# Kernel optimization log

Hardware: AMD Instinct MI355X
Metric: run time of the kernel (lower is better)

The kernel has to match this reference:

```python
import jax, jax.numpy as jnp
import numpy as np
import math

NUM_BITS = 8
EPS = 1e-5


def fake_quant(x, num_bits=NUM_BITS):
    """Uniform fake quantization over the tensor's full range (min/max), STE-friendly."""
    qmax = 2.0 ** num_bits - 1.0
    mn = jnp.min(x)
    mx = jnp.max(x)
    scale = jnp.maximum((mx - mn) / qmax, 1e-8)
    q = jnp.round(jnp.clip((x - mn) / scale, 0.0, qmax)) * scale + mn
    # straight-through estimator: forward = q, backward = identity
    return x + jax.lax.stop_gradient(q - x)


def qconv(x, w, stride, pad):
    """QConv2d: fake-quantize input (8b) and weight (8b), then fp conv (no bias)."""
    return jax.lax.conv_general_dilated(
        fake_quant(x), fake_quant(w),
        window_strides=(stride, stride),
        padding=[(pad, pad), (pad, pad)],
        dimension_numbers=("NCHW", "OIHW", "NCHW"))


def range_norm(x, gamma, beta):
    """RangeN / RangeBN (Banner et al.): per-channel mean subtraction and
    range-based scale (max-min over N,H,W) with the Gaussian range correction
    factor; affine params with 8-bit fake-quantized gamma."""
    B, C, H, W = x.shape
    n = B * H * W  # elements per channel
    scale_fix = (0.5 * 0.35) * (1.0 + (math.pi * math.log(4.0)) ** 0.5) / ((2.0 * math.log(n)) ** 0.5)
    mean = jnp.mean(x, axis=(0, 2, 3), keepdims=True)          # [1,C,1,1]
    xc = x - mean
    rng = jnp.max(xc, axis=(0, 2, 3), keepdims=True) - jnp.min(xc, axis=(0, 2, 3), keepdims=True)
    out = xc / (rng * scale_fix + EPS)
    qg = fake_quant(gamma)
    return out * qg[None, :, None, None] + beta[None, :, None, None]


def qsum(a, b):
    """Qsum: fake-quantize both addends to 8 bits, then add."""
    return fake_quant(a) + fake_quant(b)


def setup_inputs() -> dict:
    key = jax.random.key(0)
    ks = jax.random.split(key, 4)
    B, Cin, H, W = 64, 1024, 14, 14
    P = 256  # planes; expansion 4 -> Cout = 1024 == Cin (identity residual)
    x = jax.random.normal(ks[0], (B, Cin, H, W), jnp.float32)
    w1 = jax.random.normal(ks[1], (P, Cin, 1, 1), jnp.float32) * (1.0 / math.sqrt(Cin))
    w2 = jax.random.normal(ks[2], (P, P, 3, 3), jnp.float32) * (1.0 / math.sqrt(P * 9))
    w3 = jax.random.normal(ks[3], (4 * P, P, 1, 1), jnp.float32) * (1.0 / math.sqrt(P))
    g1 = jnp.ones((P,), jnp.float32); b1 = jnp.zeros((P,), jnp.float32)
    g2 = jnp.ones((P,), jnp.float32); b2 = jnp.zeros((P,), jnp.float32)
    g3 = jnp.ones((4 * P,), jnp.float32); b3 = jnp.zeros((4 * P,), jnp.float32)
    return {"x": x, "w1": w1, "g1": g1, "b1": b1, "w2": w2, "g2": g2, "b2": b2,
            "w3": w3, "g3": g3, "b3": b3}


def reference(x, w1, g1, b1, w2, g2, b2, w3, g3, b3):
    out = qconv(x, w1, stride=1, pad=0)
    out = range_norm(out, g1, b1)
    out = qconv(out, w2, stride=1, pad=1)
    out = range_norm(out, g2, b2)
    out = qconv(out, w3, stride=1, pad=0)
    out = range_norm(out, g3, b3)
    return qsum(x, out)  # downsample is None -> identity residual
```

## Files before the change

kernel.cpp:

```cpp
#include <hip/hip_runtime.h>
#include <math.h>

#ifndef M_PI
#define M_PI 3.14159265358979323846
#endif

#define NB   64
#define NCOL 12544

typedef __attribute__((ext_vector_type(4))) int int4v;

static const size_t OF_OUT = 0;
static const size_t OF_XC  = 3211264;
static const size_t OF_Z1P = 6422528;
static const size_t OF_Z2C = 7471104;
static const size_t OF_WQ1 = 8273920;
static const size_t OF_WQ2 = 8339456;
static const size_t OF_WQ3 = 8486912;
static const size_t OF_R1  = 8552448;
static const size_t OF_R2  = 8552704;
static const size_t OF_R3  = 8552960;
static const size_t OF_T2  = 8553984;
static const size_t OF_CX  = 8556032;
static const size_t OF_U2  = 8568576;
static const size_t OF_V2  = 8584960;
static const size_t OF_CZ  = 8597504;
static const size_t OF_P1  = 8610048;
static const size_t OF_P2  = 8685312;
static const size_t OF_P3  = 8760576;
static const size_t OF_PMM = 9061632;
static const size_t OF_RS  = 9064192;
static const size_t OF_ST  = 9068800;
static const size_t OF_MS  = 9068864;

__device__ __forceinline__ float fqv(float v, float mn, float sc) {
    float t = (v - mn) / sc;
    t = fminf(fmaxf(t, 0.0f), 255.0f);
    return rintf(t) * sc + mn;
}
__device__ __forceinline__ float codef(float v, float mn, float sc) {
    float t = (v - mn) / sc;
    t = fminf(fmaxf(t, 0.0f), 255.0f);
    return rintf(t) - 128.0f;
}
__device__ __forceinline__ unsigned short f2bf(float f) { return (unsigned short)(__float_as_uint(f) >> 16); }
__device__ __forceinline__ float bf2f(unsigned short u) { return __uint_as_float(((unsigned)u) << 16); }
__device__ __forceinline__ int pack4(float a, float b, float c, float d) {
    return (int)(unsigned char)(signed char)(int)a | ((int)(unsigned char)(signed char)(int)b << 8) |
           ((int)(unsigned char)(signed char)(int)c << 16) | ((int)(unsigned char)(signed char)(int)d << 24);
}
__device__ __forceinline__ void glds16(const void* g, void* l) {
    __builtin_amdgcn_global_load_lds((const __attribute__((address_space(1))) unsigned int*)g,
                                     (__attribute__((address_space(3))) unsigned int*)l, 16, 0, 0);
}

__global__ __launch_bounds__(256) void k_minmax_all(const float4* __restrict__ x, const float4* __restrict__ w1,
                                                    const float4* __restrict__ w2, const float4* __restrict__ w3,
                                                    float* __restrict__ Pmm) {
    int b = blockIdx.x;
    const float4* p; int lb, nb, n4, base;
    if (b < 1024)      { p = x;  lb = b;        nb = 1024; n4 = 3211264; base = 0; }
    else if (b < 1088) { p = w1; lb = b - 1024; nb = 64;   n4 = 65536;   base = 2048; }
    else if (b < 1216) { p = w2; lb = b - 1088; nb = 128;  n4 = 147456;  base = 2176; }
    else               { p = w3; lb = b - 1216; nb = 64;   n4 = 65536;   base = 2432; }
    float mn = INFINITY, mx = -INFINITY;
    for (int i = lb * 256 + threadIdx.x; i < n4; i += nb * 256) {
        float4 v = p[i];
        mn = fminf(mn, fminf(fminf(v.x, v.y), fminf(v.z, v.w)));
        mx = fmaxf(mx, fmaxf(fmaxf(v.x, v.y), fmaxf(v.z, v.w)));
    }
    for (int o = 32; o; o >>= 1) {
        mn = fminf(mn, __shfl_down(mn, o, 64));
        mx = fmaxf(mx, __shfl_down(mx, o, 64));
    }
    __shared__ float smn[4], smx[4];
    int lane = threadIdx.x & 63, w = threadIdx.x >> 6;
    if (lane == 0) { smn[w] = mn; smx[w] = mx; }
    __syncthreads();
    if (threadIdx.x == 0) {
        for (int i = 1; i < 4; i++) { mn = fminf(mn, smn[i]); mx = fmaxf(mx, smx[i]); }
        Pmm[base + lb * 2]     = mn;
        Pmm[base + lb * 2 + 1] = mx;
    }
}

__global__ __launch_bounds__(256) void k_fqparams2(const float* __restrict__ Pmm, float* __restrict__ sf) {
    __shared__ float sa[4], sb[4];
    int t = threadIdx.x, lane = t & 63, w = t >> 6;
    const int nbs[4]   = {1024, 64, 128, 64};
    const int bases[4] = {0, 2048, 2176, 2432};
    for (int ten = 0; ten < 4; ten++) {
        float mn = INFINITY, mx = -INFINITY;
        for (int i = t; i < nbs[ten]; i += 256) {
            mn = fminf(mn, Pmm[bases[ten] + 2 * i]);
            mx = fmaxf(mx, Pmm[bases[ten] + 2 * i + 1]);
        }
        for (int o = 32; o; o >>= 1) {
            mn = fminf(mn, __shfl_down(mn, o, 64));
            mx = fmaxf(mx, __shfl_down(mx, o, 64));
        }
        if (lane == 0) { sa[w] = mn; sb[w] = mx; }
        __syncthreads();
        if (t == 0) {
            mn = fminf(fminf(sa[0], sa[1]), fminf(sa[2], sa[3]));
            mx = fmaxf(fmaxf(sb[0], sb[1]), fmaxf(sb[2], sb[3]));
            sf[8 + 3 * ten] = mn;
            sf[9 + 3 * ten] = fmaxf((mx - mn) / 255.0f, 1e-8f);
        }
        __syncthreads();
    }
}

__global__ __launch_bounds__(256) void k_wcode_all(const float* __restrict__ w1, const float* __restrict__ w2,
                                                   const float* __restrict__ w3, const float* __restrict__ sf,
                                                   signed char* __restrict__ wq1, signed char* __restrict__ wq2,
                                                   signed char* __restrict__ wq3,
                                                   float* __restrict__ R1, float* __restrict__ R2,
                                                   float* __restrict__ R3, float* __restrict__ T8) {
    __shared__ float sh[64];
    int b = blockIdx.x, t = threadIdx.x;
    int lane = t & 63, wv = t >> 6;
    if (b < 1280) {
        const float* w; signed char* wc; float* R; int K, co; const float* pw;
        if (b < 256) { w = w1; wc = wq1; R = R1; K = 1024; co = b; pw = sf + 11; }
        else         { w = w3; wc = wq3; R = R3; K = 256;  co = b - 256; pw = sf + 17; }
        float mn = pw[0], s = pw[1];
        float sum = 0.f;
        for (int k0 = t * 4; k0 < K; k0 += 1024) {
            float4 v = *(const float4*)&w[(size_t)co * K + k0];
            float c0 = codef(v.x, mn, s), c1 = codef(v.y, mn, s), c2 = codef(v.z, mn, s), c3 = codef(v.w, mn, s);
            *(int*)&wc[(size_t)co * K + k0] = pack4(c0, c1, c2, c3);
            sum += c0 + c1 + c2 + c3;
        }
        for (int o = 32; o; o >>= 1) sum += __shfl_down(sum, o, 64);
        if (lane == 0) sh[wv] = sum;
        __syncthreads();
        if (t == 0) R[co] = sh[0] + sh[1] + sh[2] + sh[3];
    } else {
        int co = b - 1280, ci = t;
        float mn = sf[14], s = sf[15];
        float tp[9];
#pragma unroll
        for (int p = 0; p < 9; p++) {
            float c = codef(w2[((size_t)co * 256 + ci) * 9 + p], mn, s);
            wq2[(size_t)co * 2304 + p * 256 + ci] = (signed char)(int)c;
            tp[p] = c;
        }
        float* red = sh;
        float* sT = sh + 40;
#pragma unroll
        for (int p = 0; p < 9; p++) {
            float v = tp[p];
            for (int o = 32; o; o >>= 1) v += __shfl_down(v, o, 64);
            if (lane == 0) red[wv * 9 + p] = v;
        }
        __syncthreads();
        if (ci < 9) sT[ci] = red[ci] + red[9 + ci] + red[18 + ci] + red[27 + ci];
        __syncthreads();
        if (ci == 0) {
            float T0 = sT[0], T1 = sT[1], T2 = sT[2], T3 = sT[3],
                  T5 = sT[5], T6 = sT[6], T7 = sT[7], T8v = sT[8];
            R2[co] = T0 + T1 + T2 + T3 + sT[4] + T5 + T6 + T7 + T8v;
            float* o = &T8[co * 8];
            o[0] = T0 + T1 + T2;
            o[1] = T6 + T7 + T8v;
            o[2] = T0 + T3 + T6;
            o[3] = T2 + T5 + T8v;
            o[4] = T0; o[5] = T2; o[6] = T6; o[7] = T8v;
        }
    }
}

__global__ __launch_bounds__(256) void k_code0(const float* __restrict__ x, signed char* __restrict__ dst,
                                               const float* __restrict__ qp, float* __restrict__ CX) {
    __shared__ unsigned short lt[28][264];
    int n = blockIdx.z, hw0 = blockIdx.x * 28, cq = blockIdx.y * 256;
    int t = threadIdx.x;
    float qmn = qp[0], qsc = qp[1];
    const float* sp = x + ((size_t)n * 1024 + cq) * 196 + hw0;
    for (int i = t; i < 7168; i += 256) {
        int c = i / 28, hw = i - c * 28;
        lt[hw][c] = f2bf(codef(sp[(size_t)c * 196 + hw], qmn, qsc));
    }
    __syncthreads();
    int lane = t & 63, wv = t >> 6;
    int c0 = lane * 4;
#pragma unroll
    for (int s = 0; s < 7; s++) {
        int i = s * 4 + wv;
        int pk = pack4(bf2f(lt[i][c0]), bf2f(lt[i][c0 + 1]), bf2f(lt[i][c0 + 2]), bf2f(lt[i][c0 + 3]));
        *(int*)&dst[((size_t)n * 196 + hw0 + i) * 1024 + cq + c0] = pk;
    }
    for (int i = wv; i < 28; i += 4) {
        float s = bf2f(lt[i][lane]) + bf2f(lt[i][lane + 64]) +
                  bf2f(lt[i][lane + 128]) + bf2f(lt[i][lane + 192]);
        for (int o = 32; o; o >>= 1) s += __shfl_down(s, o, 64);
        if (lane == 0) atomicAdd(&CX[n * 196 + hw0 + i], s);
    }
}

template <int PAD>
__global__ __launch_bounds__(256) void k_codeE(const float* __restrict__ src, signed char* __restrict__ dst,
                                               const float* __restrict__ mean, const float* __restrict__ sg,
                                               const float* __restrict__ beta, const float* __restrict__ qp,
                                               float* __restrict__ rowsum) {
    int t = threadIdx.x, lane = t & 63, wv = t >> 6;
    int c4 = lane * 4;
    float4 m4 = *(const float4*)&mean[c4];
    float4 s4 = *(const float4*)&sg[c4];
    float4 b4 = *(const float4*)&beta[c4];
    float qmn = qp[0], qsc = qp[1];
#pragma unroll
    for (int r = 0; r < 4; r++) {
        int j = blockIdx.x * 16 + wv * 4 + r;
        float4 v = *(const float4*)&src[(size_t)j * 256 + c4];
        float c0 = codef((v.x - m4.x) * s4.x + b4.x, qmn, qsc);
        float c1 = codef((v.y - m4.y) * s4.y + b4.y, qmn, qsc);
        float c2 = codef((v.z - m4.z) * s4.z + b4.z, qmn, qsc);
        float c3 = codef((v.w - m4.w) * s4.w + b4.w, qmn, qsc);
        int n = j / 196, hw = j - n * 196, h = hw / 14, w = hw - (hw / 14) * 14;
        size_t di;
        if (PAD) di = (((size_t)n * 16 + h + 1) * 16 + (w + 1)) * 256 + c4;
        else     di = (size_t)j * 256 + c4;
        *(int*)&dst[di] = pack4(c0, c1, c2, c3);
        float s = c0 + c1 + c2 + c3;
        for (int o = 32; o; o >>= 1) s += __shfl_down(s, o, 64);
        if (lane == 0) {
            if (PAD) rowsum[((size_t)n * 16 + h + 1) * 16 + (w + 1)] = s;
            else     rowsum[j] = s;
        }
    }
}

__global__ __launch_bounds__(256) void k_v2(const float* __restrict__ U, float* __restrict__ V) {
    int j = blockIdx.x * 256 + threadIdx.x;
    if (j >= NCOL) return;
    int n = j / 196, hw = j - n * 196, h = hw / 14, w = hw - (hw / 14) * 14;
    const float* u = U + (size_t)n * 256;
    float s = 0.f;
#pragma unroll
    for (int r = 0; r < 3; r++)
#pragma unroll
        for (int c = 0; c < 3; c++) s += u[(h + r) * 16 + (w + c)];
    V[j] = s;
}

template <int MODE>
__global__ __launch_bounds__(256, 2) void k_conv12(const signed char* __restrict__ Acts,
                                                   const signed char* __restrict__ Wts,
                                                   const float* __restrict__ R, const float* __restrict__ T8,
                                                   const float* __restrict__ Cj,
                                                   const float* __restrict__ pw, const float* __restrict__ pz,
                                                   float* __restrict__ outNHWC, int K,
                                                   float* __restrict__ Ps, float* __restrict__ Pn,
                                                   float* __restrict__ Px) {
    __shared__ __align__(16) signed char As[2 * 16384];
    __shared__ __align__(16) signed char Bs[2 * 8192];
    __shared__ float Lst[2][64][3];
    int tid = threadIdx.x, lane = tid & 63, wave = tid >> 6;
    int wm = wave >> 1, wn = wave & 1;
    int jb = blockIdx.x * 128, cob = blockIdx.y * 64;
    int sr = tid >> 3, spos = tid & 7, sc = spos ^ (sr & 7);

    const signed char* aq[4];
#pragma unroll
    for (int q = 0; q < 4; q++) {
        int j = jb + q * 32 + sr;
        if (MODE == 0) aq[q] = Acts + (size_t)j * K + sc * 16;
        else {
            int n = j / 196, hw = j - n * 196, h = hw / 14, w = hw - (hw / 14) * 14;
            aq[q] = Acts + (((size_t)n * 16 + h) * 16 + w) * 256 + sc * 16;
        }
    }
    const signed char* bq[2];
#pragma unroll
    for (int q = 0; q < 2; q++) bq[q] = Wts + (size_t)(cob + q * 32 + sr) * K + sc * 16;

    int4v acc[4][2];
#pragma unroll
    for (int mi = 0; mi < 4; mi++)
#pragma unroll
        for (int ni = 0; ni < 2; ni++) acc[mi][ni] = (int4v)0;

    int nk = K >> 7;
    auto stage = [&](int b, int ks) {
        size_t koA;
        if (MODE == 0) koA = (size_t)ks << 7;
        else {
            int k = ks << 7;
            int p = k >> 8, kin = k & 255;
            int rr = p / 3, ss = p - 3 * rr;
            koA = (size_t)(rr * 16 + ss) * 256 + kin;
        }
#pragma unroll
        for (int q = 0; q < 4; q++)
            glds16(aq[q] + koA, &As[b * 16384 + (q * 32 + sr) * 128 + spos * 16]);
#pragma unroll
        for (int q = 0; q < 2; q++)
            glds16(bq[q] + ((size_t)ks << 7), &Bs[b * 8192 + (q * 32 + sr) * 128 + spos * 16]);
    };

    int l15 = lane & 15, kq = lane >> 4, sw = l15 & 7;
    stage(0, 0);
    for (int ks = 0; ks < nk; ks++) {
        __syncthreads();
        if (ks + 1 < nk) stage((ks + 1) & 1, ks + 1);
        int b = ks & 1;
#pragma unroll
        for (int kc = 0; kc < 2; kc++) {
            int col = ((kc * 4 + kq) ^ sw) << 4;
            int4v a[4], bb[2];
#pragma unroll
            for (int mi = 0; mi < 4; mi++)
                a[mi] = *(const int4v*)&As[b * 16384 + (wm * 64 + mi * 16 + l15) * 128 + col];
#pragma unroll
            for (int ni = 0; ni < 2; ni++)
                bb[ni] = *(const int4v*)&Bs[b * 8192 + (wn * 32 + ni * 16 + l15) * 128 + col];
#pragma unroll
            for (int mi = 0; mi < 4; mi++)
#pragma unroll
                for (int ni = 0; ni < 2; ni++)
                    acc[mi][ni] = __builtin_amdgcn_mfma_i32_16x16x64_i8(a[mi], bb[ni], acc[mi][ni], 0, 0, 0);
        }
    }

    float aw = pw[1], bw = pw[0] + 128.f * pw[1];
    float az = pz[1], bz = pz[0] + 128.f * pz[1];
    float caa = aw * az, cR = aw * bz, cC = bw * az, cK = bw * bz;
    int cco[2]; float rr0[2]; float t8v[2][8];
#pragma unroll
    for (int ni = 0; ni < 2; ni++) {
        cco[ni] = cob + wn * 32 + ni * 16 + l15;
        rr0[ni] = R[cco[ni]];
        if (MODE == 1) {
#pragma unroll
            for (int p = 0; p < 8; p++) t8v[ni][p] = T8[cco[ni] * 8 + p];
        }
    }
    float ssm[2] = {0.f, 0.f}, smnv[2] = {INFINITY, INFINITY}, smxv[2] = {-INFINITY, -INFINITY};
#pragma unroll
    for (int mi = 0; mi < 4; mi++)
#pragma unroll
        for (int reg = 0; reg < 4; reg++) {
            int j = jb + wm * 64 + mi * 16 + kq * 4 + reg;
            int n = j / 196, hw = j - n * 196;
            float cj = Cj[j];
            float constterm;
            float pt = 0.f, pb = 0.f, pl = 0.f, pr = 0.f, ctl = 0.f, ctr = 0.f, cbl = 0.f, cbr = 0.f;
            if (MODE == 1) {
                int h = hw / 14, w = hw - (hw / 14) * 14;
                pt = (h == 0) ? 1.f : 0.f;  pb = (h == 13) ? 1.f : 0.f;
                pl = (w == 0) ? 1.f : 0.f;  pr = (w == 13) ? 1.f : 0.f;
                ctl = pt * pl; ctr = pt * pr; cbl = pb * pl; cbr = pb * pr;
                float miss = 3.f * (pt + pb + pl + pr) - (ctl + ctr + cbl + cbr);
                constterm = cK * (256.f * (9.f - miss));
            } else {
                constterm = cK * (float)K;
            }
#pragma unroll
            for (int ni = 0; ni < 2; ni++) {
                float rsum = rr0[ni];
                if (MODE == 1)
                    rsum -= pt * t8v[ni][0] + pb * t8v[ni][1] + pl * t8v[ni][2] + pr * t8v[ni][3]
                          - ctl * t8v[ni][4] - ctr * t8v[ni][5] - cbl * t8v[ni][6] - cbr * t8v[ni][7];
                float v = caa * (float)acc[mi][ni][reg] + cR * rsum + cC * cj + constterm;
                outNHWC[(size_t)j * 256 + cco[ni]] = v;
                ssm[ni] += v;
                smnv[ni] = fminf(smnv[ni], v);
                smxv[ni] = fmaxf(smxv[ni], v);
            }
        }
#pragma unroll
    for (int ni = 0; ni < 2; ni++) {
        float s = ssm[ni], mn = smnv[ni], mx = smxv[ni];
        s += __shfl_xor(s, 16, 64); s += __shfl_xor(s, 32, 64);
        mn = fminf(mn, __shfl_xor(mn, 16, 64)); mn = fminf(mn, __shfl_xor(mn, 32, 64));
        mx = fmaxf(mx, __shfl_xor(mx, 16, 64)); mx = fmaxf(mx, __shfl_xor(mx, 32, 64));
        if (kq == 0) {
            int cl = wn * 32 + ni * 16 + l15;
            Lst[wm][cl][0] = s; Lst[wm][cl][1] = mn; Lst[wm][cl][2] = mx;
        }
    }
    __syncthreads();
    if (tid < 64) {
        float s  = Lst[0][tid][0] + Lst[1][tid][0];
        float mn = fminf(Lst[0][tid][1], Lst[1][tid][1]);
        float mx = fmaxf(Lst[0][tid][2], Lst[1][tid][2]);
        int idx = blockIdx.x * 256 + cob + tid;
        Ps[idx] = s; Pn[idx] = mn; Px[idx] = mx;
    }
}

__global__ __launch_bounds__(256, 2) void k_conv3(const signed char* __restrict__ Wts,
                                                  const signed char* __restrict__ Zc,
                                                  const float* __restrict__ R, const float* __restrict__ Cj,
                                                  const float* __restrict__ pw, const float* __restrict__ pz,
                                                  float* __restrict__ out,
                                                  float* __restrict__ Ps, float* __restrict__ Pn,
                                                  float* __restrict__ Px) {
    __shared__ __align__(16) signed char As[32768];
    __shared__ __align__(16) signed char Bs[32768];
    __shared__ float Lst[2][128][3];
    int tid = threadIdx.x, lane = tid & 63, wave = tid >> 6;
    int wm = wave >> 1, wn = wave & 1;
    int jb = blockIdx.x * 128, cob = blockIdx.y * 128;
    int sr = tid >> 4, spos = tid & 15;
#pragma unroll
    for (int p = 0; p < 8; p++) {
        int row = p * 16 + sr;
        int cg = spos ^ (row & 7);
        glds16(Zc + (size_t)(jb + row) * 256 + cg * 16, &As[p * 4096 + tid * 16]);
    }
#pragma unroll
    for (int p = 0; p < 8; p++) {
        int row = p * 16 + sr;
        int cg = spos ^ (row & 7);
        glds16(Wts + (size_t)(cob + row) * 256 + cg * 16, &Bs[p * 4096 + tid * 16]);
    }
    __syncthreads();

    int4v acc[4][4];
#pragma unroll
    for (int mi = 0; mi < 4; mi++)
#pragma unroll
        for (int ni = 0; ni < 4; ni++) acc[mi][ni] = (int4v)0;

    int l15 = lane & 15, kq = lane >> 4, sw = l15 & 7;
#pragma unroll
    for (int kc = 0; kc < 4; kc++) {
        int col = ((kc * 4 + kq) ^ sw) << 4;
        int4v a[4], bb[4];
#pragma unroll
        for (int mi = 0; mi < 4; mi++)
            a[mi] = *(const int4v*)&As[(wm * 64 + mi * 16 + l15) * 256 + col];
#pragma unroll
        for (int ni = 0; ni < 4; ni++)
            bb[ni] = *(const int4v*)&Bs[(wn * 64 + ni * 16 + l15) * 256 + col];
#pragma unroll
        for (int mi = 0; mi < 4; mi++)
#pragma unroll
            for (int ni = 0; ni < 4; ni++)
                acc[mi][ni] = __builtin_amdgcn_mfma_i32_16x16x64_i8(a[mi], bb[ni], acc[mi][ni], 0, 0, 0);
    }

    float aw = pw[1], bw = pw[0] + 128.f * pw[1];
    float az = pz[1], bz = pz[0] + 128.f * pz[1];
    float caa = aw * az, cR = aw * bz, cC = bw * az, cK = bw * bz;
    int coA[4]; float rA[4];
#pragma unroll
    for (int ni = 0; ni < 4; ni++) {
        coA[ni] = cob + wn * 64 + ni * 16 + l15;
        rA[ni] = R[coA[ni]];
    }
    float ps[4], pmn[4], pmx[4];
#pragma unroll
    for (int ni = 0; ni < 4; ni++) { ps[ni] = 0.f; pmn[ni] = INFINITY; pmx[ni] = -INFINITY; }
#pragma unroll
    for (int mi = 0; mi < 4; mi++) {
        int j0 = jb + wm * 64 + mi * 16 + kq * 4;
        int n = j0 / 196, hh = j0 - n * 196;
        float4 cj = *(const float4*)&Cj[j0];
#pragma unroll
        for (int ni = 0; ni < 4; ni++) {
            float base = cR * rA[ni] + cK * 256.f;
            float4 v;
            v.x = caa * (float)acc[mi][ni][0] + base + cC * cj.x;
            v.y = caa * (float)acc[mi][ni][1] + base + cC * cj.y;
            v.z = caa * (float)acc[mi][ni][2] + base + cC * cj.z;
            v.w = caa * (float)acc[mi][ni][3] + base + cC * cj.w;
            *(float4*)&out[((size_t)n * 1024 + coA[ni]) * 196 + hh] = v;
            ps[ni] += v.x + v.y + v.z + v.w;
            pmn[ni] = fminf(pmn[ni], fminf(fminf(v.x, v.y), fminf(v.z, v.w)));
            pmx[ni] = fmaxf(pmx[ni], fmaxf(fmaxf(v.x, v.y), fmaxf(v.z, v.w)));
        }
    }
#pragma unroll
    for (int ni = 0; ni < 4; ni++) {
        float s = ps[ni], mn = pmn[ni], mx = pmx[ni];
        s += __shfl_xor(s, 16, 64); s += __shfl_xor(s, 32, 64);
        mn = fminf(mn, __shfl_xor(mn, 16, 64)); mn = fminf(mn, __shfl_xor(mn, 32, 64));
        mx = fmaxf(mx, __shfl_xor(mx, 16, 64)); mx = fmaxf(mx, __shfl_xor(mx, 32, 64));
        if (kq == 0) {
            int cl = wn * 64 + ni * 16 + l15;
            Lst[wm][cl][0] = s; Lst[wm][cl][1] = mn; Lst[wm][cl][2] = mx;
        }
    }
    __syncthreads();
    if (tid < 128) {
        float s  = Lst[0][tid][0] + Lst[1][tid][0];
        float mn = fminf(Lst[0][tid][1], Lst[1][tid][1]);
        float mx = fmaxf(Lst[0][tid][2], Lst[1][tid][2]);
        int idx = blockIdx.x * 1024 + cob + tid;
        Ps[idx] = s; Pn[idx] = mn; Px[idx] = mx;
    }
}

__global__ __launch_bounds__(256) void k_redstats(const float* __restrict__ Ps, const float* __restrict__ Pn,
                                                  const float* __restrict__ Px, int C,
                                                  float* __restrict__ sum_o, float* __restrict__ mn_o,
                                                  float* __restrict__ mx_o) {
    __shared__ float Ls[4][64][3];
    int t = threadIdx.x, cl = t & 63, sl = t >> 6;
    int co = blockIdx.x * 64 + cl;
    float s = 0.f, mn = INFINITY, mx = -INFINITY;
    for (int b = sl; b < 98; b += 4) {
        s += Ps[b * C + co];
        mn = fminf(mn, Pn[b * C + co]);
        mx = fmaxf(mx, Px[b * C + co]);
    }
    Ls[sl][cl][0] = s; Ls[sl][cl][1] = mn; Ls[sl][cl][2] = mx;
    __syncthreads();
    if (t < 64) {
        s = Ls[0][t][0] + Ls[1][t][0] + Ls[2][t][0] + Ls[3][t][0];
        mn = fminf(fminf(Ls[0][t][1], Ls[1][t][1]), fminf(Ls[2][t][1], Ls[3][t][1]));
        mx = fmaxf(fmaxf(Ls[0][t][2], Ls[1][t][2]), fmaxf(Ls[2][t][2], Ls[3][t][2]));
        int co2 = blockIdx.x * 64 + t;
        sum_o[co2] = s; mn_o[co2] = mn; mx_o[co2] = mx;
    }
}

__global__ __launch_bounds__(256) void k_finnorm(int C, const float* __restrict__ gamma, const float* __restrict__ beta,
                                                 const float* __restrict__ sum_i, const float* __restrict__ mn_i,
                                                 const float* __restrict__ mx_i, float* mean_o, float* sg_o,
                                                 float* qp, float scale_fix) {
    int tid = threadIdx.x;
    int lane = tid & 63, w = tid >> 6;
    __shared__ float sa[4], sb[4];
    float gmn = INFINITY, gmx = -INFINITY;
    for (int c = tid; c < C; c += 256) { float g = gamma[c]; gmn = fminf(gmn, g); gmx = fmaxf(gmx, g); }
    for (int o = 32; o; o >>= 1) { gmn = fminf(gmn, __shfl_down(gmn, o, 64)); gmx = fmaxf(gmx, __shfl_down(gmx, o, 64)); }
    if (lane == 0) { sa[w] = gmn; sb[w] = gmx; }
    __syncthreads();
    gmn = fminf(fminf(sa[0], sa[1]), fminf(sa[2], sa[3]));
    gmx = fmaxf(fmaxf(sb[0], sb[1]), fmaxf(sb[2], sb[3]));
    float gsc = fmaxf((gmx - gmn) / 255.0f, 1e-8f);
    __syncthreads();
    float qmn = INFINITY, qmx = -INFINITY;
    for (int c = tid; c < C; c += 256) {
        float mean = sum_i[c] / 12544.0f;
        float cmn = mn_i[c], cmx = mx_i[c];
        float rng = cmx - cmn;
        float qg = fqv(gamma[c], gmn, gsc);
        float s = qg / (rng * scale_fix + 1e-5f);
        mean_o[c] = mean; sg_o[c] = s;
        float b = beta[c];
        float lo = (cmn - mean) * s + b;
        float hi = (cmx - mean) * s + b;
        qmn = fminf(qmn, fminf(lo, hi));
        qmx = fmaxf(qmx, fmaxf(lo, hi));
    }
    for (int o = 32; o; o >>= 1) { qmn = fminf(qmn, __shfl_down(qmn, o, 64)); qmx = fmaxf(qmx, __shfl_down(qmx, o, 64)); }
    if (lane == 0) { sa[w] = qmn; sb[w] = qmx; }
    __syncthreads();
    if (tid == 0) {
        qmn = fminf(fminf(sa[0], sa[1]), fminf(sa[2], sa[3]));
        qmx = fmaxf(fmaxf(sb[0], sb[1]), fmaxf(sb[2], sb[3]));
        qp[0] = qmn;
        qp[1] = fmaxf((qmx - qmn) / 255.0f, 1e-8f);
    }
}

__global__ __launch_bounds__(256) void k_final(const float* __restrict__ x, float* __restrict__ out,
                                               const float* __restrict__ mean, const float* __restrict__ sg,
                                               const float* __restrict__ beta, const float* __restrict__ sf,
                                               const float* __restrict__ qp) {
    float xmn = sf[8], xsc = sf[9];
    float qmn = qp[0], qsc = qp[1];
    const float4* xp = (const float4*)x;
    float4* yp = (float4*)out;
    int n4 = 12845056 / 4;
    int i = blockIdx.x * blockDim.x + threadIdx.x;
    int str = gridDim.x * blockDim.x;
    for (; i < n4; i += str) {
        int e = i * 4;
        int c = (e / 196) & 1023;
        float m = mean[c], s = sg[c], b = beta[c];
        float4 xv = xp[i], ov = yp[i], r;
        r.x = fqv(xv.x, xmn, xsc) + fqv((ov.x - m) * s + b, qmn, qsc);
        r.y = fqv(xv.y, xmn, xsc) + fqv((ov.y - m) * s + b, qmn, qsc);
        r.z = fqv(xv.z, xmn, xsc) + fqv((ov.z - m) * s + b, qmn, qsc);
        r.w = fqv(xv.w, xmn, xsc) + fqv((ov.w - m) * s + b, qmn, qsc);
        yp[i] = r;
    }
}

extern "C" void kernel_launch(void* const* d_in, const int* in_sizes, int n_in,
                              void* d_out, int out_size, void* d_ws, size_t ws_size,
                              hipStream_t stream) {
    const float* x  = (const float*)d_in[0];
    const float* w1 = (const float*)d_in[1];
    const float* g1 = (const float*)d_in[2];
    const float* b1 = (const float*)d_in[3];
    const float* w2 = (const float*)d_in[4];
    const float* g2 = (const float*)d_in[5];
    const float* b2 = (const float*)d_in[6];
    const float* w3 = (const float*)d_in[7];
    const float* g3 = (const float*)d_in[8];
    const float* b3 = (const float*)d_in[9];
    float* out = (float*)d_out;

    float* W = (float*)d_ws;
    float* OUT = W + OF_OUT;
    signed char* xc  = (signed char*)(W + OF_XC);
    signed char* z1p = (signed char*)(W + OF_Z1P);
    signed char* z2c = (signed char*)(W + OF_Z2C);
    signed char* wq1 = (signed char*)(W + OF_WQ1);
    signed char* wq2 = (signed char*)(W + OF_WQ2);
    signed char* wq3 = (signed char*)(W + OF_WQ3);
    float* R1 = W + OF_R1; float* R2 = W + OF_R2; float* R3 = W + OF_R3;
    float* T2 = W + OF_T2;
    float* CX = W + OF_CX; float* U2 = W + OF_U2; float* V2 = W + OF_V2; float* CZ = W + OF_CZ;
    float* P1s = W + OF_P1, *P1n = P1s + 25088, *P1x = P1s + 50176;
    float* P2s = W + OF_P2, *P2n = P2s + 25088, *P2x = P2s + 50176;
    float* P3s = W + OF_P3, *P3n = P3s + 100352, *P3x = P3s + 200704;
    float* Pmm = W + OF_PMM;
    float* RS = W + OF_RS;
    float* sum1 = RS, *mn1 = RS + 256, *mx1 = RS + 512;
    float* sum2 = RS + 768, *mn2 = RS + 1024, *mx2 = RS + 1280;
    float* sum3 = RS + 1536, *mn3 = RS + 2560, *mx3 = RS + 3584;
    float* S = W + OF_ST;
    float* MS = W + OF_MS;
    float* mean1 = MS, *sg1 = MS + 256, *mean2 = MS + 512, *sg2 = MS + 768, *mean3 = MS + 1024, *sg3 = MS + 2048;

    const float scale_fix =
        (float)((0.5 * 0.35) * (1.0 + sqrt(M_PI * log(4.0))) / sqrt(2.0 * log(12544.0)));

    hipMemsetAsync(CX, 0, 12544 * 4, stream);
    hipMemsetAsync(U2, 0, 16384 * 4, stream);
    hipMemsetAsync(z1p, 0, 4194304, stream);

    k_minmax_all<<<1280, 256, 0, stream>>>((const float4*)x, (const float4*)w1,
                                           (const float4*)w2, (const float4*)w3, Pmm);
    k_fqparams2<<<1, 256, 0, stream>>>(Pmm, S);

    k_wcode_all<<<1536, 256, 0, stream>>>(w1, w2, w3, S, wq1, wq2, wq3, R1, R2, R3, T2);

    k_code0<<<dim3(7, 4, 64), 256, 0, stream>>>(x, xc, S + 8, CX);

    k_conv12<0><<<dim3(98, 4), 256, 0, stream>>>(xc, wq1, R1, nullptr, CX, S + 11, S + 8, OUT, 1024,
                                                 P1s, P1n, P1x);
    k_redstats<<<4, 256, 0, stream>>>(P1s, P1n, P1x, 256, sum1, mn1, mx1);
    k_finnorm<<<1, 256, 0, stream>>>(256, g1, b1, sum1, mn1, mx1, mean1, sg1, S + 20, scale_fix);
    k_codeE<1><<<784, 256, 0, stream>>>(OUT, z1p, mean1, sg1, b1, S + 20, U2);
    k_v2<<<49, 256, 0, stream>>>(U2, V2);

    k_conv12<1><<<dim3(98, 4), 256, 0, stream>>>(z1p, wq2, R2, T2, V2, S + 14, S + 20, OUT, 2304,
                                                 P2s, P2n, P2x);
    k_redstats<<<4, 256, 0, stream>>>(P2s, P2n, P2x, 256, sum2, mn2, mx2);
    k_finnorm<<<1, 256, 0, stream>>>(256, g2, b2, sum2, mn2, mx2, mean2, sg2, S + 23, scale_fix);
    k_codeE<0><<<784, 256, 0, stream>>>(OUT, z2c, mean2, sg2, b2, S + 23, CZ);

    k_conv3<<<dim3(98, 8), 256, 0, stream>>>(wq3, z2c, R3, CZ, S + 17, S + 23, out, P3s, P3n, P3x);
    k_redstats<<<16, 256, 0, stream>>>(P3s, P3n, P3x, 1024, sum3, mn3, mx3);
    k_finnorm<<<1, 256, 0, stream>>>(1024, g3, b3, sum3, mn3, mx3, mean3, sg3, S + 26, scale_fix);
    k_final<<<2048, 256, 0, stream>>>(x, out, mean3, sg3, b3, S, S + 26);
}
```

Baseline: 281.5 us.

## Fold norm-stat reductions into conv epilogues via atomics and recompute params per block

Replaces the per-block partial-stat buffers plus the separate reduce and finalize kernels with double-precision atomic sums and order-preserving integer atomic min/max in the conv epilogues. Each consuming kernel (codeE, conv, final) recomputes the normalization and quantization parameters itself from these accumulators. The 3x3 window sum moves into the conv2 epilogue, dropping k_v2, and the memsets are folded into the first minmax kernel. This removes about ten small kernel launches and their serialization, at the cost of atomic contention and redundant per-block parameter recomputation.

```diff
diff --git a/kernel.cpp b/kernel.cpp
--- a/kernel.cpp
+++ b/kernel.cpp
@@ -23,15 +23,18 @@
 static const size_t OF_T2  = 8553984;
 static const size_t OF_CX  = 8556032;
 static const size_t OF_U2  = 8568576;
-static const size_t OF_V2  = 8584960;
 static const size_t OF_CZ  = 8597504;
-static const size_t OF_P1  = 8610048;
-static const size_t OF_P2  = 8685312;
-static const size_t OF_P3  = 8760576;
+static const size_t OF_SD1 = 8610048;
+static const size_t OF_SD2 = 8610560;
+static const size_t OF_SD3 = 8611072;
+static const size_t OF_MN1 = 8613120;
+static const size_t OF_MX1 = 8613376;
+static const size_t OF_MN2 = 8613632;
+static const size_t OF_MX2 = 8613888;
+static const size_t OF_MN3 = 8614144;
+static const size_t OF_MX3 = 8615168;
 static const size_t OF_PMM = 9061632;
-static const size_t OF_RS  = 9064192;
 static const size_t OF_ST  = 9068800;
-static const size_t OF_MS  = 9068864;
 
 __device__ __forceinline__ float fqv(float v, float mn, float sc) {
     float t = (v - mn) / sc;
@@ -53,10 +56,82 @@
     __builtin_amdgcn_global_load_lds((const __attribute__((address_space(1))) unsigned int*)g,
                                      (__attribute__((address_space(3))) unsigned int*)l, 16, 0, 0);
 }
+__device__ __forceinline__ unsigned fkey(float f) {
+    unsigned u = __float_as_uint(f);
+    return (u & 0x80000000u) ? ~u : (u | 0x80000000u);
+}
+__device__ __forceinline__ float unfkey(unsigned k) {
+    unsigned u = (k & 0x80000000u) ? (k & 0x7FFFFFFFu) : ~k;
+    return __uint_as_float(u);
+}
+
+__device__ __forceinline__ void blk_minmax(float& mn, float& mx, volatile float* scr) {
+    for (int o = 32; o; o >>= 1) {
+        mn = fminf(mn, __shfl_down(mn, o, 64));
+        mx = fmaxf(mx, __shfl_down(mx, o, 64));
+    }
+    int lane = threadIdx.x & 63, wv = threadIdx.x >> 6;
+    __syncthreads();
+    if (lane == 0) { scr[wv] = mn; scr[4 + wv] = mx; }
+    __syncthreads();
+    mn = fminf(fminf(scr[0], scr[1]), fminf(scr[2], scr[3]));
+    mx = fmaxf(fmaxf(scr[4], scr[5]), fmaxf(scr[6], scr[7]));
+}
+
+template <int C>
+__device__ void stage_params(const float* __restrict__ gamma, const float* __restrict__ beta,
+                             const double* __restrict__ sumd, const unsigned* __restrict__ mnk,
+                             const unsigned* __restrict__ mxk, float scale_fix,
+                             float* lmean, float* lsg, volatile float* scr,
+                             float& zmn, float& zsc) {
+    int t = threadIdx.x;
+    float gmn = INFINITY, gmx = -INFINITY;
+    for (int c = t; c < C; c += 256) {
+        float g = gamma[c];
+        gmn = fminf(gmn, g); gmx = fmaxf(gmx, g);
+    }
+    blk_minmax(gmn, gmx, scr);
+    float gsc = fmaxf((gmx - gmn) / 255.0f, 1e-8f);
+    float qmn = INFINITY, qmx = -INFINITY;
+    for (int c = t; c < C; c += 256) {
+        float mean = (float)sumd[c] / 12544.0f;
+        float cmn = unfkey(mnk[c]), cmx = unfkey(mxk[c]);
+        float rng = cmx - cmn;
+        float qg = fqv(gamma[c], gmn, gsc);
+        float s = qg / (rng * scale_fix + 1e-5f);
+        if (lmean) { lmean[c] = mean; lsg[c] = s; }
+        float b = beta[c];
+        float lo = (cmn - mean) * s + b;
+        float hi = (cmx - mean) * s + b;
+        qmn = fminf(qmn, fminf(lo, hi));
+        qmx = fmaxf(qmx, fmaxf(lo, hi));
+    }
+    blk_minmax(qmn, qmx, scr);
+    zmn = qmn;
+    zsc = fmaxf((qmx - qmn) / 255.0f, 1e-8f);
+}
 
 __global__ __launch_bounds__(256) void k_minmax_all(const float4* __restrict__ x, const float4* __restrict__ w1,
                                                     const float4* __restrict__ w2, const float4* __restrict__ w3,
-                                                    float* __restrict__ Pmm) {
+                                                    float* __restrict__ Pmm, float* __restrict__ Wf) {
+    {
+        unsigned g = blockIdx.x * 256 + threadIdx.x;
+        int* zp = (int*)(Wf + OF_Z1P);
+        for (unsigned i = g; i < 1048576u; i += 327680u) zp[i] = 0;
+        if (g < 12544u) Wf[OF_CX + g] = 0.0f;
+        if (g < 16384u) Wf[OF_U2 + g] = 0.0f;
+        if (g < 3072u)  ((int*)(Wf + OF_SD1))[g] = 0;
+        if (g < 256u) {
+            ((unsigned*)(Wf + OF_MN1))[g] = 0xFF800000u;
+            ((unsigned*)(Wf + OF_MX1))[g] = 0x007FFFFFu;
+            ((unsigned*)(Wf + OF_MN2))[g] = 0xFF800000u;
+            ((unsigned*)(Wf + OF_MX2))[g] = 0x007FFFFFu;
+        }
+        if (g < 1024u) {
+            ((unsigned*)(Wf + OF_MN3))[g] = 0xFF800000u;
+            ((unsigned*)(Wf + OF_MX3))[g] = 0x007FFFFFu;
+        }
+    }
     int b = blockIdx.x;
     const float4* p; int lb, nb, n4, base;
     if (b < 1024)      { p = x;  lb = b;        nb = 1024; n4 = 3211264; base = 0; }
@@ -201,15 +276,21 @@
 
 template <int PAD>
 __global__ __launch_bounds__(256) void k_codeE(const float* __restrict__ src, signed char* __restrict__ dst,
-                                               const float* __restrict__ mean, const float* __restrict__ sg,
-                                               const float* __restrict__ beta, const float* __restrict__ qp,
+                                               const float* __restrict__ gamma, const float* __restrict__ beta_g,
+                                               const double* __restrict__ sumd, const unsigned* __restrict__ mnk,
+                                               const unsigned* __restrict__ mxk, float scale_fix,
                                                float* __restrict__ rowsum) {
+    __shared__ __align__(16) float lmean[256];
+    __shared__ __align__(16) float lsg[256];
+    __shared__ float scr[8];
+    float qmn, qsc;
+    stage_params<256>(gamma, beta_g, sumd, mnk, mxk, scale_fix, lmean, lsg, scr, qmn, qsc);
+    __syncthreads();
     int t = threadIdx.x, lane = t & 63, wv = t >> 6;
     int c4 = lane * 4;
-    float4 m4 = *(const float4*)&mean[c4];
-    float4 s4 = *(const float4*)&sg[c4];
-    float4 b4 = *(const float4*)&beta[c4];
-    float qmn = qp[0], qsc = qp[1];
+    float4 m4 = *(const float4*)&lmean[c4];
+    float4 s4 = *(const float4*)&lsg[c4];
+    float4 b4 = *(const float4*)&beta_g[c4];
 #pragma unroll
     for (int r = 0; r < 4; r++) {
         int j = blockIdx.x * 16 + wv * 4 + r;
@@ -232,35 +313,31 @@
     }
 }
 
-__global__ __launch_bounds__(256) void k_v2(const float* __restrict__ U, float* __restrict__ V) {
-    int j = blockIdx.x * 256 + threadIdx.x;
-    if (j >= NCOL) return;
-    int n = j / 196, hw = j - n * 196, h = hw / 14, w = hw - (hw / 14) * 14;
-    const float* u = U + (size_t)n * 256;
-    float s = 0.f;
-#pragma unroll
-    for (int r = 0; r < 3; r++)
-#pragma unroll
-        for (int c = 0; c < 3; c++) s += u[(h + r) * 16 + (w + c)];
-    V[j] = s;
-}
-
 template <int MODE>
 __global__ __launch_bounds__(256, 2) void k_conv12(const signed char* __restrict__ Acts,
                                                    const signed char* __restrict__ Wts,
                                                    const float* __restrict__ R, const float* __restrict__ T8,
                                                    const float* __restrict__ Cj,
                                                    const float* __restrict__ pw, const float* __restrict__ pz,
+                                                   const float* __restrict__ pzg, const float* __restrict__ pzb,
+                                                   const double* __restrict__ pzsum,
+                                                   const unsigned* __restrict__ pzmn,
+                                                   const unsigned* __restrict__ pzmx, float scale_fix,
                                                    float* __restrict__ outNHWC, int K,
-                                                   float* __restrict__ Ps, float* __restrict__ Pn,
-                                                   float* __restrict__ Px) {
+                                                   double* __restrict__ Sumd, unsigned* __restrict__ Mnk,
+                                                   unsigned* __restrict__ Mxk) {
     __shared__ __align__(16) signed char As[2 * 16384];
     __shared__ __align__(16) signed char Bs[2 * 8192];
     __shared__ float Lst[2][64][3];
+    __shared__ float pscr[8];
     int tid = threadIdx.x, lane = tid & 63, wave = tid >> 6;
     int wm = wave >> 1, wn = wave & 1;
     int jb = blockIdx.x * 128, cob = blockIdx.y * 64;
     int sr = tid >> 3, spos = tid & 7, sc = spos ^ (sr & 7);
+
+    float zmn = 0.f, zsc = 0.f;
+    if (MODE == 1)
+        stage_params<256>(pzg, pzb, pzsum, pzmn, pzmx, scale_fix, nullptr, nullptr, pscr, zmn, zsc);
 
     const signed char* aq[4];
 #pragma unroll
@@ -325,7 +402,9 @@
     }
 
     float aw = pw[1], bw = pw[0] + 128.f * pw[1];
-    float az = pz[1], bz = pz[0] + 128.f * pz[1];
+    float az, bz;
+    if (MODE == 1) { az = zsc; bz = zmn + 128.f * zsc; }
+    else           { az = pz[1]; bz = pz[0] + 128.f * pz[1]; }
     float caa = aw * az, cR = aw * bz, cC = bw * az, cK = bw * bz;
     int cco[2]; float rr0[2]; float t8v[2][8];
 #pragma unroll
@@ -344,8 +423,7 @@
         for (int reg = 0; reg < 4; reg++) {
             int j = jb + wm * 64 + mi * 16 + kq * 4 + reg;
             int n = j / 196, hw = j - n * 196;
-            float cj = Cj[j];
-            float constterm;
+            float constterm, cjv;
             float pt = 0.f, pb = 0.f, pl = 0.f, pr = 0.f, ctl = 0.f, ctr = 0.f, cbl = 0.f, cbr = 0.f;
             if (MODE == 1) {
                 int h = hw / 14, w = hw - (hw / 14) * 14;
@@ -354,8 +432,11 @@
                 ctl = pt * pl; ctr = pt * pr; cbl = pb * pl; cbr = pb * pr;
                 float miss = 3.f * (pt + pb + pl + pr) - (ctl + ctr + cbl + cbr);
                 constterm = cK * (256.f * (9.f - miss));
+                const float* u = Cj + n * 256 + h * 16 + w;
+                cjv = u[0] + u[1] + u[2] + u[16] + u[17] + u[18] + u[32] + u[33] + u[34];
             } else {
                 constterm = cK * (float)K;
+                cjv = Cj[j];
             }
 #pragma unroll
             for (int ni = 0; ni < 2; ni++) {
@@ -363,7 +444,7 @@
                 if (MODE == 1)
                     rsum -= pt * t8v[ni][0] + pb * t8v[ni][1] + pl * t8v[ni][2] + pr * t8v[ni][3]
                           - ctl * t8v[ni][4] - ctr * t8v[ni][5] - cbl * t8v[ni][6] - cbr * t8v[ni][7];
-                float v = caa * (float)acc[mi][ni][reg] + cR * rsum + cC * cj + constterm;
+                float v = caa * (float)acc[mi][ni][reg] + cR * rsum + cC * cjv + constterm;
                 outNHWC[(size_t)j * 256 + cco[ni]] = v;
                 ssm[ni] += v;
                 smnv[ni] = fminf(smnv[ni], v);
@@ -386,25 +467,36 @@
         float s  = Lst[0][tid][0] + Lst[1][tid][0];
         float mn = fminf(Lst[0][tid][1], Lst[1][tid][1]);
         float mx = fmaxf(Lst[0][tid][2], Lst[1][tid][2]);
-        int idx = blockIdx.x * 256 + cob + tid;
-        Ps[idx] = s; Pn[idx] = mn; Px[idx] = mx;
+        int co = cob + tid;
+        atomicAdd(&Sumd[co], (double)s);
+        atomicMin(&Mnk[co], fkey(mn));
+        atomicMax(&Mxk[co], fkey(mx));
     }
 }
 
 __global__ __launch_bounds__(256, 2) void k_conv3(const signed char* __restrict__ Wts,
                                                   const signed char* __restrict__ Zc,
                                                   const float* __restrict__ R, const float* __restrict__ Cj,
-                                                  const float* __restrict__ pw, const float* __restrict__ pz,
+                                                  const float* __restrict__ pw,
+                                                  const float* __restrict__ pzg, const float* __restrict__ pzb,
+                                                  const double* __restrict__ pzsum,
+                                                  const unsigned* __restrict__ pzmn,
+                                                  const unsigned* __restrict__ pzmx, float scale_fix,
                                                   float* __restrict__ out,
-                                                  float* __restrict__ Ps, float* __restrict__ Pn,
-                                                  float* __restrict__ Px) {
+                                                  double* __restrict__ Sumd, unsigned* __restrict__ Mnk,
+                                                  unsigned* __restrict__ Mxk) {
     __shared__ __align__(16) signed char As[32768];
     __shared__ __align__(16) signed char Bs[32768];
     __shared__ float Lst[2][128][3];
+    __shared__ float pscr[8];
     int tid = threadIdx.x, lane = tid & 63, wave = tid >> 6;
     int wm = wave >> 1, wn = wave & 1;
     int jb = blockIdx.x * 128, cob = blockIdx.y * 128;
     int sr = tid >> 4, spos = tid & 15;
+
+    float zmn, zsc;
+    stage_params<256>(pzg, pzb, pzsum, pzmn, pzmx, scale_fix, nullptr, nullptr, pscr, zmn, zsc);
+
 #pragma unroll
     for (int p = 0; p < 8; p++) {
         int row = p * 16 + sr;
@@ -444,7 +536,7 @@
     }
 
     float aw = pw[1], bw = pw[0] + 128.f * pw[1];
-    float az = pz[1], bz = pz[0] + 128.f * pz[1];
+    float az = zsc, bz = zmn + 128.f * zsc;
     float caa = aw * az, cR = aw * bz, cC = bw * az, cK = bw * bz;
     int coA[4]; float rA[4];
 #pragma unroll
@@ -490,82 +582,25 @@
         float s  = Lst[0][tid][0] + Lst[1][tid][0];
         float mn = fminf(Lst[0][tid][1], Lst[1][tid][1]);
         float mx = fmaxf(Lst[0][tid][2], Lst[1][tid][2]);
-        int idx = blockIdx.x * 1024 + cob + tid;
-        Ps[idx] = s; Pn[idx] = mn; Px[idx] = mx;
-    }
-}
-
-__global__ __launch_bounds__(256) void k_redstats(const float* __restrict__ Ps, const float* __restrict__ Pn,
-                                                  const float* __restrict__ Px, int C,
-                                                  float* __restrict__ sum_o, float* __restrict__ mn_o,
-                                                  float* __restrict__ mx_o) {
-    __shared__ float Ls[4][64][3];
-    int t = threadIdx.x, cl = t & 63, sl = t >> 6;
-    int co = blockIdx.x * 64 + cl;
-    float s = 0.f, mn = INFINITY, mx = -INFINITY;
-    for (int b = sl; b < 98; b += 4) {
-        s += Ps[b * C + co];
-        mn = fminf(mn, Pn[b * C + co]);
-        mx = fmaxf(mx, Px[b * C + co]);
-    }
-    Ls[sl][cl][0] = s; Ls[sl][cl][1] = mn; Ls[sl][cl][2] = mx;
-    __syncthreads();
-    if (t < 64) {
-        s = Ls[0][t][0] + Ls[1][t][0] + Ls[2][t][0] + Ls[3][t][0];
-        mn = fminf(fminf(Ls[0][t][1], Ls[1][t][1]), fminf(Ls[2][t][1], Ls[3][t][1]));
-        mx = fmaxf(fmaxf(Ls[0][t][2], Ls[1][t][2]), fmaxf(Ls[2][t][2], Ls[3][t][2]));
-        int co2 = blockIdx.x * 64 + t;
-        sum_o[co2] = s; mn_o[co2] = mn; mx_o[co2] = mx;
-    }
-}
-
-__global__ __launch_bounds__(256) void k_finnorm(int C, const float* __restrict__ gamma, const float* __restrict__ beta,
-                                                 const float* __restrict__ sum_i, const float* __restrict__ mn_i,
-                                                 const float* __restrict__ mx_i, float* mean_o, float* sg_o,
-                                                 float* qp, float scale_fix) {
-    int tid = threadIdx.x;
-    int lane = tid & 63, w = tid >> 6;
-    __shared__ float sa[4], sb[4];
-    float gmn = INFINITY, gmx = -INFINITY;
-    for (int c = tid; c < C; c += 256) { float g = gamma[c]; gmn = fminf(gmn, g); gmx = fmaxf(gmx, g); }
-    for (int o = 32; o; o >>= 1) { gmn = fminf(gmn, __shfl_down(gmn, o, 64)); gmx = fmaxf(gmx, __shfl_down(gmx, o, 64)); }
-    if (lane == 0) { sa[w] = gmn; sb[w] = gmx; }
-    __syncthreads();
-    gmn = fminf(fminf(sa[0], sa[1]), fminf(sa[2], sa[3]));
-    gmx = fmaxf(fmaxf(sb[0], sb[1]), fmaxf(sb[2], sb[3]));
-    float gsc = fmaxf((gmx - gmn) / 255.0f, 1e-8f);
-    __syncthreads();
-    float qmn = INFINITY, qmx = -INFINITY;
-    for (int c = tid; c < C; c += 256) {
-        float mean = sum_i[c] / 12544.0f;
-        float cmn = mn_i[c], cmx = mx_i[c];
-        float rng = cmx - cmn;
-        float qg = fqv(gamma[c], gmn, gsc);
-        float s = qg / (rng * scale_fix + 1e-5f);
-        mean_o[c] = mean; sg_o[c] = s;
-        float b = beta[c];
-        float lo = (cmn - mean) * s + b;
-        float hi = (cmx - mean) * s + b;
-        qmn = fminf(qmn, fminf(lo, hi));
-        qmx = fmaxf(qmx, fmaxf(lo, hi));
-    }
-    for (int o = 32; o; o >>= 1) { qmn = fminf(qmn, __shfl_down(qmn, o, 64)); qmx = fmaxf(qmx, __shfl_down(qmx, o, 64)); }
-    if (lane == 0) { sa[w] = qmn; sb[w] = qmx; }
-    __syncthreads();
-    if (tid == 0) {
-        qmn = fminf(fminf(sa[0], sa[1]), fminf(sa[2], sa[3]));
-        qmx = fmaxf(fmaxf(sb[0], sb[1]), fmaxf(sb[2], sb[3]));
-        qp[0] = qmn;
-        qp[1] = fmaxf((qmx - qmn) / 255.0f, 1e-8f);
+        int co = cob + tid;
+        atomicAdd(&Sumd[co], (double)s);
+        atomicMin(&Mnk[co], fkey(mn));
+        atomicMax(&Mxk[co], fkey(mx));
     }
 }
 
 __global__ __launch_bounds__(256) void k_final(const float* __restrict__ x, float* __restrict__ out,
-                                               const float* __restrict__ mean, const float* __restrict__ sg,
-                                               const float* __restrict__ beta, const float* __restrict__ sf,
-                                               const float* __restrict__ qp) {
+                                               const float* __restrict__ gamma, const float* __restrict__ beta,
+                                               const double* __restrict__ sumd, const unsigned* __restrict__ mnk,
+                                               const unsigned* __restrict__ mxk, float scale_fix,
+                                               const float* __restrict__ sf) {
+    __shared__ float lmean[1024];
+    __shared__ float lsg[1024];
+    __shared__ float scr[8];
+    float qmn, qsc;
+    stage_params<1024>(gamma, beta, sumd, mnk, mxk, scale_fix, lmean, lsg, scr, qmn, qsc);
+    __syncthreads();
     float xmn = sf[8], xsc = sf[9];
-    float qmn = qp[0], qsc = qp[1];
     const float4* xp = (const float4*)x;
     float4* yp = (float4*)out;
     int n4 = 12845056 / 4;
@@ -574,7 +609,7 @@
     for (; i < n4; i += str) {
         int e = i * 4;
         int c = (e / 196) & 1023;
-        float m = mean[c], s = sg[c], b = beta[c];
+        float m = lmean[c], s = lsg[c], b = beta[c];
         float4 xv = xp[i], ov = yp[i], r;
         r.x = fqv(xv.x, xmn, xsc) + fqv((ov.x - m) * s + b, qmn, qsc);
         r.y = fqv(xv.y, xmn, xsc) + fqv((ov.y - m) * s + b, qmn, qsc);
@@ -609,49 +644,40 @@
     signed char* wq3 = (signed char*)(W + OF_WQ3);
     float* R1 = W + OF_R1; float* R2 = W + OF_R2; float* R3 = W + OF_R3;
     float* T2 = W + OF_T2;
-    float* CX = W + OF_CX; float* U2 = W + OF_U2; float* V2 = W + OF_V2; float* CZ = W + OF_CZ;
-    float* P1s = W + OF_P1, *P1n = P1s + 25088, *P1x = P1s + 50176;
-    float* P2s = W + OF_P2, *P2n = P2s + 25088, *P2x = P2s + 50176;
-    float* P3s = W + OF_P3, *P3n = P3s + 100352, *P3x = P3s + 200704;
+    float* CX = W + OF_CX; float* U2 = W + OF_U2; float* CZ = W + OF_CZ;
+    double* SD1 = (double*)(W + OF_SD1);
+    double* SD2 = (double*)(W + OF_SD2);
+    double* SD3 = (double*)(W + OF_SD3);
+    unsigned* MN1 = (unsigned*)(W + OF_MN1); unsigned* MX1 = (unsigned*)(W + OF_MX1);
+    unsigned* MN2 = (unsigned*)(W + OF_MN2); unsigned* MX2 = (unsigned*)(W + OF_MX2);
+    unsigned* MN3 = (unsigned*)(W + OF_MN3); unsigned* MX3 = (unsigned*)(W + OF_MX3);
     float* Pmm = W + OF_PMM;
-    float* RS = W + OF_RS;
-    float* sum1 = RS, *mn1 = RS + 256, *mx1 = RS + 512;
-    float* sum2 = RS + 768, *mn2 = RS + 1024, *mx2 = RS + 1280;
-    float* sum3 = RS + 1536, *mn3 = RS + 2560, *mx3 = RS + 3584;
     float* S = W + OF_ST;
-    float* MS = W + OF_MS;
-    float* mean1 = MS, *sg1 = MS + 256, *mean2 = MS + 512, *sg2 = MS + 768, *mean3 = MS + 1024, *sg3 = MS + 2048;
 
     const float scale_fix =
         (float)((0.5 * 0.35) * (1.0 + sqrt(M_PI * log(4.0))) / sqrt(2.0 * log(12544.0)));
 
-    hipMemsetAsync(CX, 0, 12544 * 4, stream);
-    hipMemsetAsync(U2, 0, 16384 * 4, stream);
-    hipMemsetAsync(z1p, 0, 4194304, stream);
-
     k_minmax_all<<<1280, 256, 0, stream>>>((const float4*)x, (const float4*)w1,
-                                           (const float4*)w2, (const float4*)w3, Pmm);
+                                           (const float4*)w2, (const float4*)w3, Pmm, W);
     k_fqparams2<<<1, 256, 0, stream>>>(Pmm, S);
 
     k_wcode_all<<<1536, 256, 0, stream>>>(w1, w2, w3, S, wq1, wq2, wq3, R1, R2, R3, T2);
 
     k_code0<<<dim3(7, 4, 64), 256, 0, stream>>>(x, xc, S + 8, CX);
 
-    k_conv12<0><<<dim3(98, 4), 256, 0, stream>>>(xc, wq1, R1, nullptr, CX, S + 11, S + 8, OUT, 1024,
-                                                 P1s, P1n, P1x);
-    k_redstats<<<4, 256, 0, stream>>>(P1s, P1n, P1x, 256, sum1, mn1, mx1);
-    k_finnorm<<<1, 256, 0, stream>>>(256, g1, b1, sum1, mn1, mx1, mean1, sg1, S + 20, scale_fix);
-    k_codeE<1><<<784, 256, 0, stream>>>(OUT, z1p, mean1, sg1, b1, S + 20, U2);
-    k_v2<<<49, 256, 0, stream>>>(U2, V2);
-
-    k_conv12<1><<<dim3(98, 4), 256, 0, stream>>>(z1p, wq2, R2, T2, V2, S + 14, S + 20, OUT, 2304,
-                                                 P2s, P2n, P2x);
-    k_redstats<<<4, 256, 0, stream>>>(P2s, P2n, P2x, 256, sum2, mn2, mx2);
-    k_finnorm<<<1, 256, 0, stream>>>(256, g2, b2, sum2, mn2, mx2, mean2, sg2, S + 23, scale_fix);
-    k_codeE<0><<<784, 256, 0, stream>>>(OUT, z2c, mean2, sg2, b2, S + 23, CZ);
-
-    k_conv3<<<dim3(98, 8), 256, 0, stream>>>(wq3, z2c, R3, CZ, S + 17, S + 23, out, P3s, P3n, P3x);
-    k_redstats<<<16, 256, 0, stream>>>(P3s, P3n, P3x, 1024, sum3, mn3, mx3);
-    k_finnorm<<<1, 256, 0, stream>>>(1024, g3, b3, sum3, mn3, mx3, mean3, sg3, S + 26, scale_fix);
-    k_final<<<2048, 256, 0, stream>>>(x, out, mean3, sg3, b3, S, S + 26);
-}
+    k_conv12<0><<<dim3(98, 4), 256, 0, stream>>>(xc, wq1, R1, nullptr, CX, S + 11, S + 8,
+                                                 nullptr, nullptr, nullptr, nullptr, nullptr, 0.f,
+                                                 OUT, 1024, SD1, MN1, MX1);
+    k_codeE<1><<<784, 256, 0, stream>>>(OUT, z1p, g1, b1, SD1, MN1, MX1, scale_fix, U2);
+
+    k_conv12<1><<<dim3(98, 4), 256, 0, stream>>>(z1p, wq2, R2, T2, U2, S + 14, nullptr,
+                                                 g1, b1, SD1, MN1, MX1, scale_fix,
+                                                 OUT, 2304, SD2, MN2, MX2);
+    k_codeE<0><<<784, 256, 0, stream>>>(OUT, z2c, g2, b2, SD2, MN2, MX2, scale_fix, CZ);
+
+    k_conv3<<<dim3(98, 8), 256, 0, stream>>>(wq3, z2c, R3, CZ, S + 17,
+                                             g2, b2, SD2, MN2, MX2, scale_fix,
+                                             out, SD3, MN3, MX3);
+
+    k_final<<<2048, 256, 0, stream>>>(x, out, g3, b3, SD3, MN3, MX3, scale_fix, S);
+}
```

After: 251.8 us. -10.6%, faster.
